# Kernel tuning notes

Hardware: AMD Instinct MI355X
Metric: run time of the kernel (lower is better)

The kernel has to match this reference:

```python
import jax, jax.numpy as jnp
import numpy as np

EPS = 1e-6

def _ln(x, g, b):
    m = jnp.mean(x, axis=-1, keepdims=True)
    v = jnp.mean(jnp.square(x - m), axis=-1, keepdims=True)
    return (x - m) / jnp.sqrt(v + EPS) * g + b

def setup_inputs() -> dict:
    key = jax.random.key(0)
    ks = jax.random.split(key, 16)
    B, L, D = 4, 2048, 1024
    s = 0.02
    inp = {
        'q': jax.random.normal(ks[0], (B, L, D), jnp.float32),
        'k': jax.random.normal(ks[1], (B, L, D), jnp.float32),
        'v': jax.random.normal(ks[2], (B, L, D), jnp.float32),
    }
    wnames = ['Wq1', 'Wk1', 'Wv1', 'Wf1', 'Wq2', 'Wk2', 'Wv2', 'Wf2']
    for i, n in enumerate(wnames):
        inp[n] = jax.random.normal(ks[3 + i], (D, D), jnp.float32) * s
        inp['b' + n[1:]] = jnp.zeros((D,), jnp.float32)
    for n in ['q1', 'k1', 'v1', 'q2', 'k2', 'v2']:
        inp['g' + n] = jnp.ones((D,), jnp.float32)
        inp['B' + n] = jnp.zeros((D,), jnp.float32)
    return inp

def reference(q, k, v, Wq1, bq1, Wk1, bk1, Wv1, bv1, Wf1, bf1,
              Wq2, bq2, Wk2, bk2, Wv2, bv2, Wf2, bf2,
              gq1, Bq1, gk1, Bk1, gv1, Bv1, gq2, Bq2, gk2, Bk2, gv2, Bv2):
    # n_head = 1 (forced by LayerNorm(n_head*d_k) on last dim d_k); d_k = 1024
    temp = jnp.sqrt(jnp.asarray(q.shape[-1], q.dtype))

    def attn(qi, ki, vi):
        a = jax.nn.softmax(jnp.einsum('bqd,bkd->bqk', qi / temp, ki), axis=-1)
        return jnp.einsum('bqk,bkd->bqd', a, vi), a

    # layer 1
    q1 = q @ Wq1 + bq1
    k1 = k @ Wk1 + bk1
    v1 = v @ Wv1 + bv1
    residual1 = q1
    o1, _ = attn(_ln(q1, gq1, Bq1), _ln(k1, gk1, Bk1), _ln(v1, gv1, Bv1))
    o1 = o1 @ Wf1 + bf1
    # layer 2
    q2 = o1 @ Wq2 + bq2
    k2 = k @ Wk2 + bk2
    v2 = v @ Wv2 + bv2
    residual2 = q2
    o2, a2 = attn(_ln(q2, gq2, Bq2), _ln(k2, gk2, Bk2), _ln(v2, gv2, Bv2))
    out = o2 @ Wf2 + bf2
    # residuals in torch have shape (b, l, 1, d_k); cat on last dim -> (b, l, 1, 2*d_k)
    res = jnp.concatenate([residual1, residual2], axis=-1)[:, :, None, :]
    # attn2.squeeze() drops the singleton head dim -> (b, lq, lk)
    return out, res, a2
```

## Files before the change

kernel.cpp:

```cpp
#include <hip/hip_runtime.h>

#define DEV __device__ __forceinline__

using short8  = __attribute__((ext_vector_type(8))) short;
using floatx4 = __attribute__((ext_vector_type(4))) float;

DEV unsigned short f2bf(float f) {
  unsigned int u = __float_as_uint(f);
  u += 0x7FFFu + ((u >> 16) & 1u);
  return (unsigned short)(u >> 16);
}
DEV float bf2f(unsigned short u) { return __uint_as_float(((unsigned int)u) << 16); }

DEV void stage16(void* lds, const void* g) {
  __builtin_amdgcn_global_load_lds(
      (__attribute__((address_space(1))) void*)g,
      (__attribute__((address_space(3))) void*)lds, 16, 0, 0);
}

DEV float wave_sum(float x) {
#pragma unroll
  for (int m = 32; m; m >>= 1) x += __shfl_xor(x, m);
  return x;
}
DEV float wave_max(float x) {
#pragma unroll
  for (int m = 32; m; m >>= 1) x = fmaxf(x, __shfl_xor(x, m));
  return x;
}

DEV void g128_core(const short* __restrict__ A, const short* __restrict__ Bt,
                   const float* __restrict__ bias,
                   float* __restrict__ Cf, unsigned short* __restrict__ Cb,
                   float* __restrict__ C2, int offc2,
                   int N, int K, int m0, int n0) {
  __shared__ __align__(16) short lds[4][8192];

  const int t    = threadIdx.x;
  const int lane = t & 63;
  const int w    = t >> 6;
  const int wm   = w >> 1;
  const int wn   = w & 1;
  const int NT   = K >> 5;

  const int isB  = w >> 1;
  const int row0 = (isB ? n0 : m0) + (w & 1) * 64 + (lane >> 2);
  const int csw  = ((lane & 3) * 8) ^ ((lane >> 5) << 4);
  const short* gbase = isB ? Bt : A;
  const short* gp[4];
#pragma unroll
  for (int i = 0; i < 4; ++i)
    gp[i] = gbase + (size_t)(row0 + i * 16) * K + csw;
  const int ldst = isB * 4096 + (w & 1) * 2048 + lane * 8;

  auto stage = [&](int tt) {
    short* dst = &lds[tt & 3][ldst];
    const int go = tt * 32;
#pragma unroll
    for (int i = 0; i < 4; ++i)
      stage16(dst + i * 512, gp[i] + go);
  };

  floatx4 acc[4][4];
#pragma unroll
  for (int i = 0; i < 4; ++i)
#pragma unroll
    for (int j = 0; j < 4; ++j)
      acc[i][j] = (floatx4){0.f, 0.f, 0.f, 0.f};

  stage(0); stage(1); stage(2);

  const int mr = lane & 15, q = lane >> 4;
  const int fo = mr * 32 + ((q * 8) ^ ((mr & 8) << 1));

  for (int kt = 0; kt < NT; ++kt) {
    asm volatile("s_waitcnt lgkmcnt(0)" ::: "memory");
    const int rem = NT - 1 - kt;
    if (rem >= 2)      asm volatile("s_waitcnt vmcnt(8)" ::: "memory");
    else if (rem == 1) asm volatile("s_waitcnt vmcnt(4)" ::: "memory");
    else               asm volatile("s_waitcnt vmcnt(0)" ::: "memory");
    __builtin_amdgcn_s_barrier();
    __builtin_amdgcn_sched_barrier(0);

    if (kt + 3 < NT) stage(kt + 3);

    const short* bufA = &lds[kt & 3][wm * 2048];
    const short* bufB = &lds[kt & 3][4096 + wn * 2048];
    short8 a[4], b[4];
#pragma unroll
    for (int m = 0; m < 4; ++m) a[m] = *(const short8*)&bufA[m * 512 + fo];
#pragma unroll
    for (int n = 0; n < 4; ++n) b[n] = *(const short8*)&bufB[n * 512 + fo];

    __builtin_amdgcn_s_setprio(1);
#pragma unroll
    for (int m = 0; m < 4; ++m)
#pragma unroll
      for (int n = 0; n < 4; ++n)
        acc[m][n] = __builtin_amdgcn_mfma_f32_16x16x32_bf16(a[m], b[n], acc[m][n], 0, 0, 0);
    __builtin_amdgcn_s_setprio(0);
  }

#pragma unroll
  for (int m = 0; m < 4; ++m) {
#pragma unroll
    for (int r = 0; r < 4; ++r) {
      const int row = m0 + wm * 64 + m * 16 + q * 4 + r;
#pragma unroll
      for (int n = 0; n < 4; ++n) {
        const int col = n0 + wn * 64 + n * 16 + mr;
        float vv = acc[m][n][r];
        if (bias) vv += bias[col];
        if (Cf) Cf[(size_t)row * N + col] = vv;
        if (Cb) Cb[(size_t)row * N + col] = f2bf(vv);
        if (C2) C2[(size_t)row * 2048 + offc2 + col] = vv;
      }
    }
  }
}

DEV void xcd_decode(int gx, int gy, int& bx, int& by, int& bz) {
  const int nwg = gx * gy * gridDim.z;
  int bid = ((int)blockIdx.z * gy + (int)blockIdx.y) * gx + (int)blockIdx.x;
  const int qq = nwg >> 3, rr = nwg & 7;
  const int xcd = bid & 7, jj = bid >> 3;
  bid = (xcd < rr ? xcd * (qq + 1) : rr * (qq + 1) + (xcd - rr) * qq) + jj;
  bx = bid % gx;
  const int tmp = bid / gx;
  by = tmp % gy;
  bz = tmp / gy;
}

__global__ __launch_bounds__(256)
void g128_bt(const short* __restrict__ A, long long sAz,
             const short* __restrict__ Bt, long long sBz,
             const float* __restrict__ bias,
             float* __restrict__ Cf, long long sCfz,
             unsigned short* __restrict__ Cb, long long sCbz,
             float* __restrict__ C2, int offc2,
             int N, int K) {
  int bx, by, bz;
  xcd_decode(gridDim.x, gridDim.y, bx, by, bz);
  g128_core(A + (long long)bz * sAz, Bt + (long long)bz * sBz, bias,
            Cf ? Cf + (long long)bz * sCfz : (float*)0,
            Cb ? Cb + (long long)bz * sCbz : (unsigned short*)0,
            C2, offc2, N, K, by * 128, bx * 128);
}

struct ProjJob {
  const short* A;
  const short* Bt;
  const float* bias;
  unsigned short* Cb;
  float* C2;
  long long offc2;
};
struct Proj5 { ProjJob j[5]; };

__global__ __launch_bounds__(256)
void g128_proj5(Proj5 p) {
  int bx, by, bz;
  xcd_decode(gridDim.x, gridDim.y, bx, by, bz);
  ProjJob jb = p.j[0];
#pragma unroll
  for (int i = 1; i < 5; ++i)
    if (bz == i) jb = p.j[i];
  g128_core(jb.A, jb.Bt, jb.bias, (float*)0, jb.Cb, jb.C2, (int)jb.offc2,
            1024, 1024, by * 128, bx * 128);
}

struct LnJob {
  const unsigned short* x;
  const float* bias;
  const float* g;
  const float* Bb;
  unsigned short* y;
  float scale;
};

__global__ __launch_bounds__(256)
void ln_multi(LnJob j0, LnJob j1, LnJob j2, LnJob j3, LnJob j4) {
  LnJob jb = j0;
  if (blockIdx.y == 1) jb = j1;
  else if (blockIdx.y == 2) jb = j2;
  else if (blockIdx.y == 3) jb = j3;
  else if (blockIdx.y == 4) jb = j4;
  const int row = blockIdx.x, t = threadIdx.x;
  const ushort4 xv = ((const ushort4*)(jb.x + (size_t)row * 1024))[t];
  float4 v = {bf2f(xv.x), bf2f(xv.y), bf2f(xv.z), bf2f(xv.w)};
  if (jb.bias) {
    const float4 b4 = ((const float4*)jb.bias)[t];
    v.x += b4.x; v.y += b4.y; v.z += b4.z; v.w += b4.w;
  }
  float s  = v.x + v.y + v.z + v.w;
  float s2 = v.x * v.x + v.y * v.y + v.z * v.z + v.w * v.w;
  s = wave_sum(s);
  s2 = wave_sum(s2);
  __shared__ float r1[4], r2[4];
  const int w = t >> 6, lane = t & 63;
  if (!lane) { r1[w] = s; r2[w] = s2; }
  __syncthreads();
  s  = r1[0] + r1[1] + r1[2] + r1[3];
  s2 = r2[0] + r2[1] + r2[2] + r2[3];
  const float mean = s * (1.f / 1024.f);
  const float var  = s2 * (1.f / 1024.f) - mean * mean;
  const float rstd = 1.f / sqrtf(var + 1e-6f);
  const float4 g4 = ((const float4*)jb.g)[t];
  const float4 b4 = ((const float4*)jb.Bb)[t];
  ushort4 o;
  o.x = f2bf(((v.x - mean) * rstd * g4.x + b4.x) * jb.scale);
  o.y = f2bf(((v.y - mean) * rstd * g4.y + b4.y) * jb.scale);
  o.z = f2bf(((v.z - mean) * rstd * g4.z + b4.z) * jb.scale);
  o.w = f2bf(((v.w - mean) * rstd * g4.w + b4.w) * jb.scale);
  ((ushort4*)(jb.y + (size_t)row * 1024))[t] = o;
}

__global__ __launch_bounds__(256)
void softmax_kernel(const float* __restrict__ S, unsigned short* __restrict__ P,
                    float* __restrict__ A2) {
  const int row = blockIdx.x, t = threadIdx.x;
  const float4* sr = (const float4*)(S + (size_t)row * 2048);
  float4 a = sr[t], b = sr[t + 256];
  float m = fmaxf(fmaxf(fmaxf(a.x, a.y), fmaxf(a.z, a.w)),
                  fmaxf(fmaxf(b.x, b.y), fmaxf(b.z, b.w)));
  m = wave_max(m);
  __shared__ float red[4];
  const int w = t >> 6, lane = t & 63;
  if (!lane) red[w] = m;
  __syncthreads();
  m = fmaxf(fmaxf(red[0], red[1]), fmaxf(red[2], red[3]));
  a.x = __expf(a.x - m); a.y = __expf(a.y - m); a.z = __expf(a.z - m); a.w = __expf(a.w - m);
  b.x = __expf(b.x - m); b.y = __expf(b.y - m); b.z = __expf(b.z - m); b.w = __expf(b.w - m);
  float s = a.x + a.y + a.z + a.w + b.x + b.y + b.z + b.w;
  s = wave_sum(s);
  __syncthreads();
  if (!lane) red[w] = s;
  __syncthreads();
  s = red[0] + red[1] + red[2] + red[3];
  const float inv = 1.f / s;
  a.x *= inv; a.y *= inv; a.z *= inv; a.w *= inv;
  b.x *= inv; b.y *= inv; b.z *= inv; b.w *= inv;
  ushort4 o0, o1;
  o0.x = f2bf(a.x); o0.y = f2bf(a.y); o0.z = f2bf(a.z); o0.w = f2bf(a.w);
  o1.x = f2bf(b.x); o1.y = f2bf(b.y); o1.z = f2bf(b.z); o1.w = f2bf(b.w);
  ((ushort4*)(P + (size_t)row * 2048))[t] = o0;
  ((ushort4*)(P + (size_t)row * 2048))[t + 256] = o1;
  if (A2) {
    float4* ar = (float4*)(A2 + (size_t)row * 2048);
    ar[t] = a;
    ar[t + 256] = b;
  }
}

__global__ __launch_bounds__(256)
void cast3_kernel(const float* __restrict__ x0, const float* __restrict__ x1,
                  const float* __restrict__ x2, unsigned short* __restrict__ y0,
                  unsigned short* __restrict__ y1, unsigned short* __restrict__ y2) {
  const float* x = blockIdx.y == 0 ? x0 : (blockIdx.y == 1 ? x1 : x2);
  unsigned short* y = blockIdx.y == 0 ? y0 : (blockIdx.y == 1 ? y1 : y2);
  const int i = blockIdx.x * 256 + threadIdx.x;
  const float4 v = ((const float4*)x)[i];
  ushort4 o;
  o.x = f2bf(v.x); o.y = f2bf(v.y); o.z = f2bf(v.z); o.w = f2bf(v.w);
  ((ushort4*)y)[i] = o;
}

struct W8 {
  const float* src[8];
  unsigned short* dst[8];
};

__global__ __launch_bounds__(256)
void transpose_w8_kernel(W8 p) {
  __shared__ unsigned short tile[64][65];
  const float* in = p.src[blockIdx.z];
  unsigned short* out = p.dst[blockIdx.z];
  const int tr0 = blockIdx.y * 64, tc0 = blockIdx.x * 64;
  const int x = threadIdx.x & 63, y = threadIdx.x >> 6;
#pragma unroll
  for (int i = 0; i < 16; ++i) {
    const int r = i * 4 + y;
    tile[r][x] = f2bf(in[(size_t)(tr0 + r) * 1024 + tc0 + x]);
  }
  __syncthreads();
#pragma unroll
  for (int i = 0; i < 16; ++i) {
    const int r = i * 4 + y;
    out[(size_t)(tc0 + r) * 1024 + tr0 + x] = tile[x][r];
  }
}

__global__ __launch_bounds__(256)
void transpose_v8_kernel(const unsigned short* __restrict__ in0,
                         const unsigned short* __restrict__ in1,
                         unsigned short* __restrict__ out0,
                         unsigned short* __restrict__ out1) {
  __shared__ unsigned short tile[64][65];
  const int zz = blockIdx.z & 3;
  const unsigned short* in = (blockIdx.z < 4 ? in0 : in1) + (size_t)zz * 2048 * 1024;
  unsigned short* out = (blockIdx.z < 4 ? out0 : out1) + (size_t)zz * 1024 * 2048;
  const int tr0 = blockIdx.y * 64, tc0 = blockIdx.x * 64;
  const int x = threadIdx.x & 63, y = threadIdx.x >> 6;
#pragma unroll
  for (int i = 0; i < 16; ++i) {
    const int r = i * 4 + y;
    tile[r][x] = in[(size_t)(tr0 + r) * 1024 + tc0 + x];
  }
  __syncthreads();
#pragma unroll
  for (int i = 0; i < 16; ++i) {
    const int r = i * 4 + y;
    out[(size_t)(tc0 + r) * 2048 + tr0 + x] = tile[x][r];
  }
}

extern "C" void kernel_launch(void* const* d_in, const int* in_sizes, int n_in,
                              void* d_out, int out_size, void* d_ws, size_t ws_size,
                              hipStream_t stream) {
  const float* q = (const float*)d_in[0];
  const float* k = (const float*)d_in[1];
  const float* v = (const float*)d_in[2];
  const float* W[8];
  const float* bW[8];
  for (int i = 0; i < 8; ++i) {
    W[i]  = (const float*)d_in[3 + 2 * i];
    bW[i] = (const float*)d_in[4 + 2 * i];
  }
  const float* g_[6];
  const float* B_[6];
  for (int i = 0; i < 6; ++i) {
    g_[i] = (const float*)d_in[19 + 2 * i];
    B_[i] = (const float*)d_in[20 + 2 * i];
  }

  float* out_p = (float*)d_out;
  float* res_p = out_p + 8388608;
  float* a2_p  = res_p + 16777216;

  char* ws = (char*)d_ws;
  const size_t MBy = 1u << 20;
  unsigned short* WT   = (unsigned short*)ws;
  unsigned short* qb   = (unsigned short*)(ws + 16 * MBy);
  unsigned short* kb   = (unsigned short*)(ws + 32 * MBy);
  unsigned short* vb   = (unsigned short*)(ws + 48 * MBy);
  unsigned short* pb   = (unsigned short*)(ws + 64 * MBy);
  float* Sbuf          = (float*)(ws + 64 * MBy);
  unsigned short* lnq  = (unsigned short*)(ws + 144 * MBy);
  unsigned short* lnk1 = (unsigned short*)(ws + 160 * MBy);
  unsigned short* lnk2 = (unsigned short*)(ws + 176 * MBy);
  unsigned short* lnv1 = (unsigned short*)(ws + 192 * MBy);
  unsigned short* lnv2 = (unsigned short*)(ws + 208 * MBy);
  unsigned short* lnvT1= (unsigned short*)(ws + 224 * MBy);
  unsigned short* lnvT2= (unsigned short*)(ws + 240 * MBy);
  unsigned short* P    = (unsigned short*)(ws + 256 * MBy);
  unsigned short* ofb  = (unsigned short*)(ws + 290 * MBy);
  unsigned short* ob   = (unsigned short*)(ws + 306 * MBy);
  unsigned short* qf2b = (unsigned short*)(ws + 322 * MBy);

  const size_t SL = 8192ull * 1024;

  auto gemm = [&](const unsigned short* A, long long sAz,
                  const unsigned short* Bt, long long sBz, const float* bias,
                  float* Cf, long long sCfz, unsigned short* Cb, long long sCbz,
                  float* C2, int offc2, int M, int N, int K, int Z) {
    dim3 grid(N / 128, M / 128, Z);
    g128_bt<<<grid, 256, 0, stream>>>((const short*)A, sAz, (const short*)Bt, sBz,
                                      bias, Cf, sCfz, Cb, sCbz, C2, offc2, N, K);
  };
  LnJob nil{};

  cast3_kernel<<<dim3(8192, 3), 256, 0, stream>>>(q, k, v, qb, kb, vb);
  W8 w8;
  for (int i = 0; i < 8; ++i) { w8.src[i] = W[i]; w8.dst[i] = WT + (size_t)i * 1048576; }
  transpose_w8_kernel<<<dim3(16, 16, 8), 256, 0, stream>>>(w8);

  {
    Proj5 p;
    p.j[0] = {(const short*)kb, (const short*)(WT + 1u * 1048576), 0, pb + 0 * SL, 0, 0};
    p.j[1] = {(const short*)kb, (const short*)(WT + 5u * 1048576), 0, pb + 1 * SL, 0, 0};
    p.j[2] = {(const short*)vb, (const short*)(WT + 2u * 1048576), 0, pb + 2 * SL, 0, 0};
    p.j[3] = {(const short*)vb, (const short*)(WT + 6u * 1048576), 0, pb + 3 * SL, 0, 0};
    p.j[4] = {(const short*)qb, (const short*)(WT + 0u * 1048576), bW[0], pb + 4 * SL, res_p, 0};
    g128_proj5<<<dim3(8, 64, 5), 256, 0, stream>>>(p);
  }

  {
    LnJob jk1{pb + 0 * SL, bW[1], g_[1], B_[1], lnk1, 1.f};
    LnJob jk2{pb + 1 * SL, bW[5], g_[4], B_[4], lnk2, 1.f};
    LnJob jv1{pb + 2 * SL, bW[2], g_[2], B_[2], lnv1, 1.f};
    LnJob jv2{pb + 3 * SL, bW[6], g_[5], B_[5], lnv2, 1.f};
    LnJob jq1{pb + 4 * SL, 0,     g_[0], B_[0], lnq,  1.f / 32.f};
    ln_multi<<<dim3(8192, 5), 256, 0, stream>>>(jk1, jk2, jv1, jv2, jq1);
  }
  transpose_v8_kernel<<<dim3(16, 32, 8), 256, 0, stream>>>(lnv1, lnv2, lnvT1, lnvT2);

  gemm(lnq, 2048ll * 1024, lnk1, 2048ll * 1024, 0, Sbuf, 2048ll * 2048, 0, 0, 0, 0,
       2048, 2048, 1024, 4);
  softmax_kernel<<<8192, 256, 0, stream>>>(Sbuf, P, (float*)0);
  gemm(P, 2048ll * 2048, lnvT1, 1024ll * 2048, 0, 0, 0, ob, 2048ll * 1024, 0, 0,
       2048, 1024, 2048, 4);
  gemm(ob, 0, WT + 3u * 1048576, 0, bW[3], 0, 0, ofb, 0, 0, 0, 8192, 1024, 1024, 1);

  gemm(ofb, 0, WT + 4u * 1048576, 0, bW[4], 0, 0, qf2b, 0, res_p, 1024, 8192, 1024, 1024, 1);
  {
    LnJob jq2{qf2b, 0, g_[3], B_[3], lnq, 1.f / 32.f};
    ln_multi<<<dim3(8192, 1), 256, 0, stream>>>(jq2, nil, nil, nil, nil);
  }
  gemm(lnq, 2048ll * 1024, lnk2, 2048ll * 1024, 0, Sbuf, 2048ll * 2048, 0, 0, 0, 0,
       2048, 2048, 1024, 4);
  softmax_kernel<<<8192, 256, 0, stream>>>(Sbuf, P, a2_p);
  gemm(P, 2048ll * 2048, lnvT2, 1024ll * 2048, 0, 0, 0, ob, 2048ll * 1024, 0, 0,
       2048, 1024, 2048, 4);
  gemm(ob, 0, WT + 7u * 1048576, 0, bW[7], out_p, 0, 0, 0, 0, 0, 8192, 1024, 1024, 1);
}
```

Measured before the change: 862.8 us.

## Replace 128x128 GEMM with 256x256 tile, 8-wave, phased LDS pipeline

Rewrites the bf16 MFMA GEMM core to compute 256x256 output tiles with 512 threads, each wave owning a 128x64 slice and K stepped in chunks of 64. Global-to-LDS staging is double-buffered in 128KB of dynamic shared memory and interleaved with eight MFMA phases per iteration, each fenced by barriers. The aim is higher arithmetic intensity per byte loaded and better overlap of loads with matrix math. In exchange it needs many more accumulator registers and much more LDS, which lowers occupancy, and it launches fewer blocks for the smaller GEMMs.

```diff
diff --git a/kernel.cpp b/kernel.cpp
--- a/kernel.cpp
+++ b/kernel.cpp
@@ -29,87 +29,137 @@
   return x;
 }
 
-DEV void g128_core(const short* __restrict__ A, const short* __restrict__ Bt,
+extern __shared__ char smem[];
+
+#define MFB(va, vb, vc) __builtin_amdgcn_mfma_f32_16x16x32_bf16(va, vb, vc, 0, 0, 0)
+#define LD8(boff) (*(const short8*)(smem + (boff)))
+
+#define RDB(KC, BUF)                                   \
+  b0 = LD8((BUF) + bof + 0 * 2048 + (KC) * 1024);      \
+  b1 = LD8((BUF) + bof + 1 * 2048 + (KC) * 1024);      \
+  b2 = LD8((BUF) + bof + 2 * 2048 + (KC) * 1024);      \
+  b3 = LD8((BUF) + bof + 3 * 2048 + (KC) * 1024);
+
+#define RDA(FB, KC, BUF)                                     \
+  a0 = LD8((BUF) + aof + ((FB) + 0) * 2048 + (KC) * 1024);   \
+  a1 = LD8((BUF) + aof + ((FB) + 1) * 2048 + (KC) * 1024);   \
+  a2 = LD8((BUF) + aof + ((FB) + 2) * 2048 + (KC) * 1024);   \
+  a3 = LD8((BUF) + aof + ((FB) + 3) * 2048 + (KC) * 1024);
+
+#define STG(CLS, MT)                                                         \
+  do { const int m_ = (MT);                                                  \
+    if (m_ >= 2 && m_ < NT2) {                                               \
+      const short* rp_ = ((CLS) & 2) ? (((CLS) & 1) ? rpAhi : rpAlo)         \
+                                     : (((CLS) & 1) ? rpBhi : rpBlo);        \
+      rp_ += (size_t)m_ * 64;                                                \
+      char* d_ = lds_st + ((m_ & 1) << 16) + (((CLS) & 2) ? 0 : 32768)       \
+                 + (((CLS) & 1) ? 16384 : 0);                                \
+      stage16(d_, rp_);                                                      \
+      stage16(d_ + 1024, rp_ + 32);                                          \
+    } } while (0)
+
+#define MM(FB)                                                                                 \
+  acc[(FB)+0][0] = MFB(a0, b0, acc[(FB)+0][0]); acc[(FB)+0][1] = MFB(a0, b1, acc[(FB)+0][1]);  \
+  acc[(FB)+0][2] = MFB(a0, b2, acc[(FB)+0][2]); acc[(FB)+0][3] = MFB(a0, b3, acc[(FB)+0][3]);  \
+  acc[(FB)+1][0] = MFB(a1, b0, acc[(FB)+1][0]); acc[(FB)+1][1] = MFB(a1, b1, acc[(FB)+1][1]);  \
+  acc[(FB)+1][2] = MFB(a1, b2, acc[(FB)+1][2]); acc[(FB)+1][3] = MFB(a1, b3, acc[(FB)+1][3]);  \
+  acc[(FB)+2][0] = MFB(a2, b0, acc[(FB)+2][0]); acc[(FB)+2][1] = MFB(a2, b1, acc[(FB)+2][1]);  \
+  acc[(FB)+2][2] = MFB(a2, b2, acc[(FB)+2][2]); acc[(FB)+2][3] = MFB(a2, b3, acc[(FB)+2][3]);  \
+  acc[(FB)+3][0] = MFB(a3, b0, acc[(FB)+3][0]); acc[(FB)+3][1] = MFB(a3, b1, acc[(FB)+3][1]);  \
+  acc[(FB)+3][2] = MFB(a3, b2, acc[(FB)+3][2]); acc[(FB)+3][3] = MFB(a3, b3, acc[(FB)+3][3]);
+
+#define BARRIER   __builtin_amdgcn_s_barrier()
+#define SCHEDB    __builtin_amdgcn_sched_barrier(0)
+#define LGKM0     asm volatile("s_waitcnt lgkmcnt(0)" ::: "memory")
+
+#define PHASE_MID(FB)                 \
+  BARRIER; LGKM0; SCHEDB;             \
+  __builtin_amdgcn_s_setprio(1);      \
+  MM(FB);                             \
+  __builtin_amdgcn_s_setprio(0);
+
+#define PHASE_END BARRIER; SCHEDB;
+
+DEV void g256_core(const short* __restrict__ A, const short* __restrict__ Bt,
                    const float* __restrict__ bias,
                    float* __restrict__ Cf, unsigned short* __restrict__ Cb,
                    float* __restrict__ C2, int offc2,
                    int N, int K, int m0, int n0) {
-  __shared__ __align__(16) short lds[4][8192];
-
-  const int t    = threadIdx.x;
-  const int lane = t & 63;
-  const int w    = t >> 6;
-  const int wm   = w >> 1;
-  const int wn   = w & 1;
-  const int NT   = K >> 5;
-
-  const int isB  = w >> 1;
-  const int row0 = (isB ? n0 : m0) + (w & 1) * 64 + (lane >> 2);
-  const int csw  = ((lane & 3) * 8) ^ ((lane >> 5) << 4);
-  const short* gbase = isB ? Bt : A;
-  const short* gp[4];
-#pragma unroll
-  for (int i = 0; i < 4; ++i)
-    gp[i] = gbase + (size_t)(row0 + i * 16) * K + csw;
-  const int ldst = isB * 4096 + (w & 1) * 2048 + lane * 8;
-
-  auto stage = [&](int tt) {
-    short* dst = &lds[tt & 3][ldst];
-    const int go = tt * 32;
-#pragma unroll
-    for (int i = 0; i < 4; ++i)
-      stage16(dst + i * 512, gp[i] + go);
-  };
-
-  floatx4 acc[4][4];
-#pragma unroll
-  for (int i = 0; i < 4; ++i)
+  const int tid  = threadIdx.x;
+  const int lane = tid & 63;
+  const int w    = tid >> 6;
+  const int wm   = w >> 2;
+  const int wn   = w & 3;
+  const int mr   = lane & 15;
+  const int q    = lane >> 4;
+  const int NT2  = K >> 6;
+
+  const int srow = lane >> 2;
+  const int csw  = ((lane & 3) * 8) ^ (((lane >> 5) & 1) << 4);
+  const short* rpAlo = A  + (size_t)(m0 + w * 16 + srow) * K + csw;
+  const short* rpBlo = Bt + (size_t)(n0 + w * 16 + srow) * K + csw;
+  const short* rpAhi = rpAlo + (size_t)128 * K;
+  const short* rpBhi = rpBlo + (size_t)128 * K;
+  char* lds_st = smem + (w * 2) * 1024 + lane * 16;
+
+  const int fo  = mr * 64 + ((q * 16) ^ (((mr >> 3) & 1) << 5));
+  const int aof = wm * 16384 + fo;
+  const int bof = 32768 + wn * 8192 + fo;
+
+  floatx4 acc[8][4];
+#pragma unroll
+  for (int i = 0; i < 8; ++i)
 #pragma unroll
     for (int j = 0; j < 4; ++j)
       acc[i][j] = (floatx4){0.f, 0.f, 0.f, 0.f};
 
-  stage(0); stage(1); stage(2);
-
-  const int mr = lane & 15, q = lane >> 4;
-  const int fo = mr * 32 + ((q * 8) ^ ((mr & 8) << 1));
-
-  for (int kt = 0; kt < NT; ++kt) {
-    asm volatile("s_waitcnt lgkmcnt(0)" ::: "memory");
-    const int rem = NT - 1 - kt;
-    if (rem >= 2)      asm volatile("s_waitcnt vmcnt(8)" ::: "memory");
-    else if (rem == 1) asm volatile("s_waitcnt vmcnt(4)" ::: "memory");
-    else               asm volatile("s_waitcnt vmcnt(0)" ::: "memory");
-    __builtin_amdgcn_s_barrier();
-    __builtin_amdgcn_sched_barrier(0);
-
-    if (kt + 3 < NT) stage(kt + 3);
-
-    const short* bufA = &lds[kt & 3][wm * 2048];
-    const short* bufB = &lds[kt & 3][4096 + wn * 2048];
-    short8 a[4], b[4];
-#pragma unroll
-    for (int m = 0; m < 4; ++m) a[m] = *(const short8*)&bufA[m * 512 + fo];
-#pragma unroll
-    for (int n = 0; n < 4; ++n) b[n] = *(const short8*)&bufB[n * 512 + fo];
-
-    __builtin_amdgcn_s_setprio(1);
-#pragma unroll
-    for (int m = 0; m < 4; ++m)
-#pragma unroll
-      for (int n = 0; n < 4; ++n)
-        acc[m][n] = __builtin_amdgcn_mfma_f32_16x16x32_bf16(a[m], b[n], acc[m][n], 0, 0, 0);
-    __builtin_amdgcn_s_setprio(0);
-  }
-
-#pragma unroll
-  for (int m = 0; m < 4; ++m) {
+#pragma unroll
+  for (int mm = 0; mm < 2; ++mm) {
+    { char* d = lds_st + (mm << 16) + 32768;         const short* rp = rpBlo + mm * 64; stage16(d, rp); stage16(d + 1024, rp + 32); }
+    { char* d = lds_st + (mm << 16) + 32768 + 16384; const short* rp = rpBhi + mm * 64; stage16(d, rp); stage16(d + 1024, rp + 32); }
+    { char* d = lds_st + (mm << 16);                 const short* rp = rpAlo + mm * 64; stage16(d, rp); stage16(d + 1024, rp + 32); }
+    { char* d = lds_st + (mm << 16) + 16384;         const short* rp = rpAhi + mm * 64; stage16(d, rp); stage16(d + 1024, rp + 32); }
+  }
+  asm volatile("s_waitcnt vmcnt(8)" ::: "memory");
+  BARRIER; SCHEDB;
+
+  short8 a0, a1, a2, a3, b0, b1, b2, b3;
+
+#pragma unroll 1
+  for (int kt2 = 0; kt2 < NT2; kt2 += 2) {
+    RDB(0, 0) RDA(0, 0, 0) STG(1, kt2 + 1);
+    PHASE_MID(0) PHASE_END
+    RDA(4, 0, 0) STG(2, kt2 + 1);
+    PHASE_MID(4) PHASE_END
+    RDB(1, 0) RDA(0, 1, 0) STG(3, kt2 + 1);
+    PHASE_MID(0) PHASE_END
+    RDA(4, 1, 0) STG(0, kt2 + 2);
+    PHASE_MID(4)
+    if (kt2 + 2 < NT2) { asm volatile("s_waitcnt vmcnt(2)" ::: "memory"); }
+    else               { asm volatile("s_waitcnt vmcnt(0)" ::: "memory"); }
+    PHASE_END
+    RDB(0, 65536) RDA(0, 0, 65536) STG(1, kt2 + 2);
+    PHASE_MID(0) PHASE_END
+    RDA(4, 0, 65536) STG(2, kt2 + 2);
+    PHASE_MID(4) PHASE_END
+    RDB(1, 65536) RDA(0, 1, 65536) STG(3, kt2 + 2);
+    PHASE_MID(0) PHASE_END
+    RDA(4, 1, 65536) STG(0, kt2 + 3);
+    PHASE_MID(4)
+    if (kt2 + 3 < NT2) { asm volatile("s_waitcnt vmcnt(2)" ::: "memory"); }
+    else               { asm volatile("s_waitcnt vmcnt(0)" ::: "memory"); }
+    PHASE_END
+  }
+
+#pragma unroll
+  for (int fr = 0; fr < 8; ++fr) {
 #pragma unroll
     for (int r = 0; r < 4; ++r) {
-      const int row = m0 + wm * 64 + m * 16 + q * 4 + r;
+      const int row = m0 + wm * 128 + fr * 16 + q * 4 + r;
 #pragma unroll
       for (int n = 0; n < 4; ++n) {
         const int col = n0 + wn * 64 + n * 16 + mr;
-        float vv = acc[m][n][r];
+        float vv = acc[fr][n][r];
         if (bias) vv += bias[col];
         if (Cf) Cf[(size_t)row * N + col] = vv;
         if (Cb) Cb[(size_t)row * N + col] = f2bf(vv);
@@ -131,8 +181,8 @@
   bz = tmp / gy;
 }
 
-__global__ __launch_bounds__(256)
-void g128_bt(const short* __restrict__ A, long long sAz,
+__global__ __launch_bounds__(512, 2)
+void g256_bt(const short* __restrict__ A, long long sAz,
              const short* __restrict__ Bt, long long sBz,
              const float* __restrict__ bias,
              float* __restrict__ Cf, long long sCfz,
@@ -141,10 +191,10 @@
              int N, int K) {
   int bx, by, bz;
   xcd_decode(gridDim.x, gridDim.y, bx, by, bz);
-  g128_core(A + (long long)bz * sAz, Bt + (long long)bz * sBz, bias,
+  g256_core(A + (long long)bz * sAz, Bt + (long long)bz * sBz, bias,
             Cf ? Cf + (long long)bz * sCfz : (float*)0,
             Cb ? Cb + (long long)bz * sCbz : (unsigned short*)0,
-            C2, offc2, N, K, by * 128, bx * 128);
+            C2, offc2, N, K, by * 256, bx * 256);
 }
 
 struct ProjJob {
@@ -157,16 +207,16 @@
 };
 struct Proj5 { ProjJob j[5]; };
 
-__global__ __launch_bounds__(256)
-void g128_proj5(Proj5 p) {
+__global__ __launch_bounds__(512, 2)
+void g256_proj5(Proj5 p) {
   int bx, by, bz;
   xcd_decode(gridDim.x, gridDim.y, bx, by, bz);
   ProjJob jb = p.j[0];
 #pragma unroll
   for (int i = 1; i < 5; ++i)
     if (bz == i) jb = p.j[i];
-  g128_core(jb.A, jb.Bt, jb.bias, (float*)0, jb.Cb, jb.C2, (int)jb.offc2,
-            1024, 1024, by * 128, bx * 128);
+  g256_core(jb.A, jb.Bt, jb.bias, (float*)0, jb.Cb, jb.C2, (int)jb.offc2,
+            1024, 1024, by * 256, bx * 256);
 }
 
 struct LnJob {
@@ -331,6 +381,15 @@
   for (int i = 0; i < 6; ++i) {
     g_[i] = (const float*)d_in[19 + 2 * i];
     B_[i] = (const float*)d_in[20 + 2 * i];
+  }
+
+  static bool attr_done = false;
+  if (!attr_done) {
+    hipFuncSetAttribute((const void*)g256_bt,
+                        hipFuncAttributeMaxDynamicSharedMemorySize, 131072);
+    hipFuncSetAttribute((const void*)g256_proj5,
+                        hipFuncAttributeMaxDynamicSharedMemorySize, 131072);
+    attr_done = true;
   }
 
   float* out_p = (float*)d_out;
@@ -363,9 +422,9 @@
                   const unsigned short* Bt, long long sBz, const float* bias,
                   float* Cf, long long sCfz, unsigned short* Cb, long long sCbz,
                   float* C2, int offc2, int M, int N, int K, int Z) {
-    dim3 grid(N / 128, M / 128, Z);
-    g128_bt<<<grid, 256, 0, stream>>>((const short*)A, sAz, (const short*)Bt, sBz,
-                                      bias, Cf, sCfz, Cb, sCbz, C2, offc2, N, K);
+    dim3 grid(N / 256, M / 256, Z);
+    g256_bt<<<grid, 512, 131072, stream>>>((const short*)A, sAz, (const short*)Bt, sBz,
+                                           bias, Cf, sCfz, Cb, sCbz, C2, offc2, N, K);
   };
   LnJob nil{};
 
@@ -381,7 +440,7 @@
     p.j[2] = {(const short*)vb, (const short*)(WT + 2u * 1048576), 0, pb + 2 * SL, 0, 0};
     p.j[3] = {(const short*)vb, (const short*)(WT + 6u * 1048576), 0, pb + 3 * SL, 0, 0};
     p.j[4] = {(const short*)qb, (const short*)(WT + 0u * 1048576), bW[0], pb + 4 * SL, res_p, 0};
-    g128_proj5<<<dim3(8, 64, 5), 256, 0, stream>>>(p);
+    g256_proj5<<<dim3(4, 32, 5), 512, 131072, stream>>>(p);
   }
 
   {
```

Measured after the change: 915.9 us. +6.1%, slower.
